# Kernel tuning notes

Measured on AMD Instinct MI355X. Metric: run time of the kernel, lower is better.

The kernel has to match this reference:

```python
import jax, jax.numpy as jnp
import numpy as np

N_HEADS = 16
D_HEAD = 64  # embed_dim // n_heads = 1024 // 16


def setup_inputs() -> dict:
    key = jax.random.key(0)
    ks = jax.random.split(key, 8)
    B, S, E = 2, 2048, 1024
    return {
        "k_in": jax.random.normal(ks[0], (B, S, E), jnp.float32),
        "q_in": jax.random.normal(ks[1], (B, S, E), jnp.float32),
        "v_in": jax.random.normal(ks[2], (B, S, E), jnp.float32),
        "Wq": jax.random.normal(ks[3], (D_HEAD, D_HEAD), jnp.float32) / np.sqrt(D_HEAD),
        "Wk": jax.random.normal(ks[4], (D_HEAD, D_HEAD), jnp.float32) / np.sqrt(D_HEAD),
        "Wv": jax.random.normal(ks[5], (D_HEAD, D_HEAD), jnp.float32) / np.sqrt(D_HEAD),
        "Wo": jax.random.normal(ks[6], (E, E), jnp.float32) / np.sqrt(E),
        "bo": jnp.zeros((E,), jnp.float32),
    }


def reference(k_in, q_in, v_in, Wq, Wk, Wv, Wo, bo):
    B, Sq, E = q_in.shape
    Sk = k_in.shape[1]
    H, Dh = N_HEADS, D_HEAD
    # split heads: [B, S, H, Dh]
    q = q_in.reshape(B, Sq, H, Dh)
    k = k_in.reshape(B, Sk, H, Dh)
    v = v_in.reshape(B, Sk, H, Dh)
    # per-head linear projections (nn.Linear: x @ W.T), then [B, H, S, Dh]
    q = jnp.einsum("bshd,ed->bhse", q, Wq)
    k = jnp.einsum("bshd,ed->bhse", k, Wk)
    v = jnp.einsum("bshd,ed->bhse", v, Wv)
    # scaled dot-product attention
    scores = jnp.einsum("bhqd,bhkd->bhqk", q, k) / jnp.sqrt(jnp.asarray(Dh, q.dtype))
    attn = jax.nn.softmax(scores, axis=-1)
    ctx = jnp.einsum("bhqk,bhkd->bqhd", attn, v)  # [B, Sq, H, Dh]
    concat = ctx.reshape(B, Sq, H * Dh)
    return concat @ Wo.T + bo
```

## Files before the change

kernel.cpp:

```cpp
#include <hip/hip_runtime.h>
#include <hip/hip_fp16.h>

typedef _Float16 f16;
typedef __fp16 hf16x2 __attribute__((ext_vector_type(2)));
typedef _Float16 f16x8 __attribute__((ext_vector_type(8)));
typedef _Float16 f16x4v __attribute__((ext_vector_type(4)));
typedef float f32x4 __attribute__((ext_vector_type(4)));
typedef float f32x16 __attribute__((ext_vector_type(16)));

#define B_ 2
#define S_ 2048
#define E_ 1024
#define H_ 16
#define DH_ 64

__device__ __forceinline__ f32x4 mfma16(f16x8 a, f16x8 b, f32x4 c) {
    return __builtin_amdgcn_mfma_f32_16x16x32_f16(a, b, c, 0, 0, 0);
}
__device__ __forceinline__ f32x16 mfma32(f16x8 a, f16x8 b, f32x16 c) {
    return __builtin_amdgcn_mfma_f32_32x32x16_f16(a, b, c, 0, 0, 0);
}

__device__ __forceinline__ f16x8 cvt8(const float* p) {
    float4 v0 = *(const float4*)p;
    float4 v1 = *(const float4*)(p + 4);
    f16x8 r;
    r[0] = (f16)v0.x; r[1] = (f16)v0.y; r[2] = (f16)v0.z; r[3] = (f16)v0.w;
    r[4] = (f16)v1.x; r[5] = (f16)v1.y; r[6] = (f16)v1.z; r[7] = (f16)v1.w;
    return r;
}

__global__ __launch_bounds__(256) void proj_cvt_kernel(
    const float* __restrict__ q_in, const float* __restrict__ k_in,
    const float* __restrict__ v_in,
    const float* __restrict__ Wq, const float* __restrict__ Wk,
    const float* __restrict__ Wv, const float* __restrict__ Wo,
    f16* __restrict__ Qg, f16* __restrict__ Kg, f16* __restrict__ Vt,
    f16* __restrict__ WoH)
{
    int tid = threadIdx.x;
    int bx = blockIdx.x;
    if (bx >= 3072) {
        int i = (bx - 3072) * 256 + tid;
        float4 v = *(const float4*)(Wo + (size_t)i * 4);
        f16x4v o;
        o[0] = (f16)v.x; o[1] = (f16)v.y; o[2] = (f16)v.z; o[3] = (f16)v.w;
        *(f16x4v*)(WoH + (size_t)i * 4) = o;
        return;
    }

    int lane = tid & 63, wv = tid >> 6;
    int wid = bx * 4 + wv;
    int proj = wid >> 12;
    int r = wid & 4095;
    int bh = r >> 7;
    int stile = r & 127;
    int sbase = stile * 16;
    int h = bh & 15;
    int b = bh >> 4;
    int c = lane & 15, g = lane >> 4;

    const float* x; const float* W;
    if (proj == 0)      { x = q_in; W = Wq; }
    else if (proj == 1) { x = k_in; W = Wk; }
    else                { x = v_in; W = Wv; }

    const float* xrow = x + (((size_t)(b * S_ + sbase + c) * H_ + h) << 6);
    f16x8 a0 = cvt8(xrow + g * 8);
    f16x8 a1 = cvt8(xrow + 32 + g * 8);

    f32x4 acc[4] = {};
#pragma unroll
    for (int nt = 0; nt < 4; ++nt) {
        const float* wrow = W + ((nt * 16 + c) << 6);
        f16x8 b0 = cvt8(wrow + g * 8);
        f16x8 b1 = cvt8(wrow + 32 + g * 8);
        acc[nt] = mfma16(a0, b0, acc[nt]);
        acc[nt] = mfma16(a1, b1, acc[nt]);
    }

    if (proj < 2) {
        f16* out = (proj == 0) ? Qg : Kg;
#pragma unroll
        for (int nt = 0; nt < 4; ++nt)
#pragma unroll
            for (int j = 0; j < 4; ++j) {
                int s = sbase + g * 4 + j;
                out[((size_t)bh * S_ + s) * DH_ + nt * 16 + c] = (f16)acc[nt][j];
            }
    } else {
#pragma unroll
        for (int nt = 0; nt < 4; ++nt) {
            f16x4v pk;
            pk[0] = (f16)acc[nt][0]; pk[1] = (f16)acc[nt][1];
            pk[2] = (f16)acc[nt][2]; pk[3] = (f16)acc[nt][3];
            *(f16x4v*)&Vt[((size_t)bh * DH_ + nt * 16 + c) * S_ + sbase + g * 4] = pk;
        }
    }
}

#define C1_ 0.18033688011112042f

__global__ __launch_bounds__(256, 2) void attn_kernel(
    const f16* __restrict__ Qg, const f16* __restrict__ Kg,
    const f16* __restrict__ Vt, f16* __restrict__ ctx)
{
    __shared__ __align__(16) f16 lds[16384];

    int tid = threadIdx.x, lane = tid & 63, wv = tid >> 6;
    int bid = blockIdx.x;
    int sb = (bid & 7) * 64 + (bid >> 3);
    int bh = sb >> 4, qt = sb & 15;
    int b = bh >> 4, h = bh & 15;
    int qbase = qt * 128 + wv * 32;
    int q32 = lane & 31, hh = lane >> 5;
    bool isLo = (hh == 0);

    const f16* Qh = Qg + (size_t)bh * S_ * DH_;
    const f16* Kh = Kg + (size_t)bh * S_ * DH_;
    const f16* Vh = Vt + (size_t)bh * DH_ * S_;

    int swzr = (q32 & 15) << 3;
    int cr[8];
#pragma unroll
    for (int a = 0; a < 2; ++a)
#pragma unroll
        for (int s = 0; s < 4; ++s)
            cr[4 * a + s] = q32 * 128 + ((a * 64 + 16 * s + 8 * hh) ^ swzr);

    int s0 = tid, s1 = tid + 256;
    int e0 = s0 >> 3, c0 = s0 & 7, e1 = s1 >> 3, c1 = s1 & 7;
    int wd0 = (e0 & 31) * 128 + ((((e0 >> 5) * 64) + c0 * 8) ^ (((e0 & 31) & 15) << 3));
    int wd1 = (e1 & 31) * 128 + ((((e1 >> 5) * 64) + c1 * 8) ^ (((e1 & 31) & 15) << 3));
    const f16* ksp0 = Kh + e0 * 64 + c0 * 8;
    const f16* ksp1 = Kh + e1 * 64 + c1 * 8;
    const f16* vsp0 = Vh + (size_t)e0 * S_ + c0 * 8;
    const f16* vsp1 = Vh + (size_t)e1 * S_ + c1 * 8;

    f16x8 qf[4];
#pragma unroll
    for (int s = 0; s < 4; ++s)
        qf[s] = *(const f16x8*)(Qh + (size_t)(qbase + q32) * DH_ + 16 * s + 8 * hh);

    float m2 = -1e30f, lrv = 0.f;
    f32x16 accO0 = {}, accO1 = {};
    f16x8 kreg0, kreg1, vreg0, vreg1;

    kreg0 = *(const f16x8*)ksp0; kreg1 = *(const f16x8*)ksp1;
    vreg0 = *(const f16x8*)vsp0; vreg1 = *(const f16x8*)vsp1;
    *(f16x8*)&lds[wd0] = kreg0; *(f16x8*)&lds[wd1] = kreg1;
    *(f16x8*)&lds[8192 + wd0] = vreg0; *(f16x8*)&lds[8192 + wd1] = vreg1;
    __syncthreads();

#define ATTN_SUB(CUR, SUBI)                                                    \
    do {                                                                       \
        f32x16 accS = {};                                                      \
        __builtin_amdgcn_s_setprio(1);                                         \
        _Pragma("unroll")                                                      \
        for (int s = 0; s < 4; ++s) {                                          \
            f16x8 kf = *(const f16x8*)&lds[(CUR) * 4096 + cr[4 * (SUBI) + s]]; \
            accS = mfma32(kf, qf[s], accS);                                    \
        }                                                                      \
        __builtin_amdgcn_s_setprio(0);                                         \
        float rmax = accS[0];                                                  \
        _Pragma("unroll")                                                      \
        for (int r = 1; r < 16; ++r) rmax = fmaxf(rmax, accS[r]);              \
        rmax = fmaxf(rmax, __shfl_xor(rmax, 32));                              \
        if (!__all(fmaf(rmax, C1_, -m2) <= 8.f)) {                             \
            float mn = fmaxf(m2, rmax * C1_);                                  \
            float al = exp2f(m2 - mn);                                         \
            m2 = mn; lrv *= al;                                                \
            _Pragma("unroll")                                                  \
            for (int r = 0; r < 16; ++r) {                                     \
                float aj = __shfl(al, ((r & 3) + 8 * (r >> 2)) + 4 * hh);      \
                accO0[r] *= aj; accO1[r] *= aj;                                \
            }                                                                  \
        }                                                                      \
        unsigned w[8];                                                         \
        _Pragma("unroll")                                                      \
        for (int j = 0; j < 8; ++j) {                                          \
            float ea = exp2f(fmaf(accS[2 * j], C1_, -m2));                     \
            float eb = exp2f(fmaf(accS[2 * j + 1], C1_, -m2));                 \
            lrv += ea + eb;                                                    \
            hf16x2 pk = __builtin_amdgcn_cvt_pkrtz(ea, eb);                    \
            w[j] = __builtin_bit_cast(unsigned, pk);                           \
        }                                                                      \
        _Pragma("unroll")                                                      \
        for (int s2 = 0; s2 < 2; ++s2) {                                       \
            unsigned b0 = w[4 * s2 + 0], b1 = w[4 * s2 + 1];                   \
            unsigned b2 = w[4 * s2 + 2], b3 = w[4 * s2 + 3];                   \
            unsigned x0 = (unsigned)__shfl_xor((int)b0, 32);                   \
            unsigned x1 = (unsigned)__shfl_xor((int)b1, 32);                   \
            unsigned x2 = (unsigned)__shfl_xor((int)b2, 32);                   \
            unsigned x3 = (unsigned)__shfl_xor((int)b3, 32);                   \
            uint4 au;                                                          \
            au.x = isLo ? b0 : x2;                                             \
            au.y = isLo ? b1 : x3;                                             \
            au.z = isLo ? x0 : b2;                                             \
            au.w = isLo ? x1 : b3;                                             \
            f16x8 pa = __builtin_bit_cast(f16x8, au);                          \
            __builtin_amdgcn_s_setprio(1);                                     \
            {                                                                  \
                f16x8 vb = *(const f16x8*)&lds[8192 + (CUR) * 4096             \
                                               + cr[(SUBI) * 2 + s2]];         \
                accO0 = mfma32(pa, vb, accO0);                                 \
            }                                                                  \
            {                                                                  \
                f16x8 vb = *(const f16x8*)&lds[8192 + (CUR) * 4096             \
                                               + cr[4 + (SUBI) * 2 + s2]];     \
                accO1 = mfma32(pa, vb, accO1);                                 \
            }                                                                  \
            __builtin_amdgcn_s_setprio(0);                                     \
        }                                                                      \
    } while (0)

#define ATTN_STEP(CUR, T, STAGE)                                               \
    do {                                                                       \
        if (STAGE) {                                                           \
            kreg0 = *(const f16x8*)(ksp0 + ((T) + 1) * 4096);                  \
            kreg1 = *(const f16x8*)(ksp1 + ((T) + 1) * 4096);                  \
            vreg0 = *(const f16x8*)(vsp0 + ((T) + 1) * 64);                    \
            vreg1 = *(const f16x8*)(vsp1 + ((T) + 1) * 64);                    \
        }                                                                      \
        ATTN_SUB(CUR, 0);                                                      \
        ATTN_SUB(CUR, 1);                                                      \
        if (STAGE) {                                                           \
            int nb = (CUR) ^ 1;                                                \
            *(f16x8*)&lds[nb * 4096 + wd0] = kreg0;                            \
            *(f16x8*)&lds[nb * 4096 + wd1] = kreg1;                            \
            *(f16x8*)&lds[8192 + nb * 4096 + wd0] = vreg0;                     \
            *(f16x8*)&lds[8192 + nb * 4096 + wd1] = vreg1;                     \
            __syncthreads();                                                   \
        }                                                                      \
    } while (0)

#pragma unroll 1
    for (int kt = 0; kt < 30; kt += 2) {
        ATTN_STEP(0, kt, 1);
        ATTN_STEP(1, kt + 1, 1);
    }
    ATTN_STEP(0, 30, 1);
    ATTN_STEP(1, 31, 0);
#undef ATTN_STEP
#undef ATTN_SUB

    float lr = lrv + __shfl_xor(lrv, 32);
    float inv = 1.f / lr;
#pragma unroll
    for (int r = 0; r < 16; ++r) {
        int crow = (r & 3) + 8 * (r >> 2);
        float ir = __shfl(inv, crow + 4 * hh);
        int s = qbase + crow + 4 * hh;
        f16* dst = ctx + ((size_t)b * S_ + s) * E_ + h * DH_ + q32;
        dst[0]  = (f16)(accO0[r] * ir);
        dst[32] = (f16)(accO1[r] * ir);
    }
}

__global__ __launch_bounds__(256) void gemm_out(
    const f16* __restrict__ A,
    const f16* __restrict__ Bw,
    const float* __restrict__ bo,
    float* __restrict__ out)
{
    __shared__ __align__(16) f16 Al[2][128 * 64];
    __shared__ __align__(16) f16 Bl[2][64 * 64];

    int tid = threadIdx.x, lane = tid & 63, wv = tid >> 6;
    int bid = blockIdx.x;
    int sb = (bid & 7) * 64 + (bid >> 3);
    int mbase = (sb & 31) * 128, nbase = (sb >> 5) * 64;
    int c = lane & 15, g = lane >> 4;
    int wr = wv >> 1, wc = wv & 1;
    int swz = (c & 7) << 3;

    int adst[4]; const f16* asrc[4];
#pragma unroll
    for (int i = 0; i < 4; ++i) {
        int slot = tid + i * 256;
        int row = slot >> 3, cc = slot & 7;
        adst[i] = row * 64 + ((cc * 8) ^ ((row & 7) << 3));
        asrc[i] = A + (size_t)(mbase + row) * 1024 + cc * 8;
    }
    int bdst[2]; const f16* bsrc[2];
#pragma unroll
    for (int i = 0; i < 2; ++i) {
        int slot = tid + i * 256;
        int row = slot >> 3, cc = slot & 7;
        bdst[i] = row * 64 + ((cc * 8) ^ ((row & 7) << 3));
        bsrc[i] = Bw + (size_t)(nbase + row) * 1024 + cc * 8;
    }

    f32x4 acc[4][2] = {};
    f16x8 areg[4], breg[2];

#pragma unroll
    for (int i = 0; i < 4; ++i) areg[i] = *(const f16x8*)asrc[i];
#pragma unroll
    for (int i = 0; i < 2; ++i) breg[i] = *(const f16x8*)bsrc[i];
#pragma unroll
    for (int i = 0; i < 4; ++i) *(f16x8*)&Al[0][adst[i]] = areg[i];
#pragma unroll
    for (int i = 0; i < 2; ++i) *(f16x8*)&Bl[0][bdst[i]] = breg[i];
    __syncthreads();

#define GEMM_STEP(CUR, T, STAGE)                                               \
    do {                                                                       \
        if (STAGE) {                                                           \
            _Pragma("unroll")                                                  \
            for (int i = 0; i < 4; ++i)                                        \
                areg[i] = *(const f16x8*)(asrc[i] + ((T) + 1) * 64);           \
            _Pragma("unroll")                                                  \
            for (int i = 0; i < 2; ++i)                                        \
                breg[i] = *(const f16x8*)(bsrc[i] + ((T) + 1) * 64);           \
        }                                                                      \
        __builtin_amdgcn_s_setprio(1);                                         \
        _Pragma("unroll")                                                      \
        for (int kk = 0; kk < 2; ++kk) {                                       \
            f16x8 af[4], bf[2];                                                \
            _Pragma("unroll")                                                  \
            for (int mi = 0; mi < 4; ++mi)                                     \
                af[mi] = *(const f16x8*)&Al[CUR][(wr * 64 + mi * 16 + c) * 64  \
                                               + ((32 * kk + 8 * g) ^ swz)];   \
            _Pragma("unroll")                                                  \
            for (int ni = 0; ni < 2; ++ni)                                     \
                bf[ni] = *(const f16x8*)&Bl[CUR][(wc * 32 + ni * 16 + c) * 64  \
                                               + ((32 * kk + 8 * g) ^ swz)];   \
            _Pragma("unroll")                                                  \
            for (int mi = 0; mi < 4; ++mi)                                     \
                _Pragma("unroll")                                              \
                for (int ni = 0; ni < 2; ++ni)                                 \
                    acc[mi][ni] = mfma16(af[mi], bf[ni], acc[mi][ni]);         \
        }                                                                      \
        __builtin_amdgcn_s_setprio(0);                                         \
        if (STAGE) {                                                           \
            int nb = (CUR) ^ 1;                                                \
            _Pragma("unroll")                                                  \
            for (int i = 0; i < 4; ++i) *(f16x8*)&Al[nb][adst[i]] = areg[i];   \
            _Pragma("unroll")                                                  \
            for (int i = 0; i < 2; ++i) *(f16x8*)&Bl[nb][bdst[i]] = breg[i];   \
            __syncthreads();                                                   \
        }                                                                      \
    } while (0)

#pragma unroll 1
    for (int ks = 0; ks < 14; ks += 2) {
        GEMM_STEP(0, ks, 1);
        GEMM_STEP(1, ks + 1, 1);
    }
    GEMM_STEP(0, 14, 1);
    GEMM_STEP(1, 15, 0);
#undef GEMM_STEP

#pragma unroll
    for (int ni = 0; ni < 2; ++ni) {
        float bias = bo[nbase + wc * 32 + ni * 16 + c];
#pragma unroll
        for (int mi = 0; mi < 4; ++mi)
#pragma unroll
            for (int j = 0; j < 4; ++j) {
                int m = mbase + wr * 64 + mi * 16 + g * 4 + j;
                out[(size_t)m * 1024 + nbase + wc * 32 + ni * 16 + c] =
                    acc[mi][ni][j] + bias;
            }
    }
}

extern "C" void kernel_launch(void* const* d_in, const int* in_sizes, int n_in,
                              void* d_out, int out_size, void* d_ws, size_t ws_size,
                              hipStream_t stream)
{
    const float* k_in = (const float*)d_in[0];
    const float* q_in = (const float*)d_in[1];
    const float* v_in = (const float*)d_in[2];
    const float* Wq   = (const float*)d_in[3];
    const float* Wk   = (const float*)d_in[4];
    const float* Wv   = (const float*)d_in[5];
    const float* Wo   = (const float*)d_in[6];
    const float* bo   = (const float*)d_in[7];
    float* out = (float*)d_out;

    char* ws = (char*)d_ws;
    f16* Qg  = (f16*)(ws);
    f16* Kg  = (f16*)(ws + (8u << 20));
    f16* Vt  = (f16*)(ws + (16u << 20));
    f16* ctx = (f16*)(ws + (24u << 20));
    f16* WoH = (f16*)(ws + (32u << 20));

    proj_cvt_kernel<<<dim3(4096), dim3(256), 0, stream>>>(
        q_in, k_in, v_in, Wq, Wk, Wv, Wo, Qg, Kg, Vt, WoH);
    attn_kernel<<<dim3(512), dim3(256), 0, stream>>>(Qg, Kg, Vt, ctx);
    gemm_out<<<dim3(512), dim3(256), 0, stream>>>(ctx, WoH, bo, out);
}
```

Measured before the change: 118.6 us.

## Batch both QK^T sub-tiles before softmax and coalesce Q/K stores via LDS

The attention step now issues the QK^T MFMAs for both 32-key sub-tiles back to back and computes both row maxima together, before running softmax and PV for each. This gives the scheduler more independent MFMA work to overlap with the exp and shuffle sequences, at the cost of holding a second 16-float score accumulator in registers. Separately, the projection kernel stages Q and K results through a small per-wave LDS tile so each lane writes 16-byte contiguous rows instead of scattered 2-byte stores.

```diff
diff --git a/kernel.cpp b/kernel.cpp
--- a/kernel.cpp
+++ b/kernel.cpp
@@ -38,6 +38,8 @@
     f16* __restrict__ Qg, f16* __restrict__ Kg, f16* __restrict__ Vt,
     f16* __restrict__ WoH)
 {
+    __shared__ __align__(16) f16 tr[4][16 * 72];
+
     int tid = threadIdx.x;
     int bx = blockIdx.x;
     if (bx >= 3072) {
@@ -56,8 +58,6 @@
     int bh = r >> 7;
     int stile = r & 127;
     int sbase = stile * 16;
-    int h = bh & 15;
-    int b = bh >> 4;
     int c = lane & 15, g = lane >> 4;
 
     const float* x; const float* W;
@@ -65,36 +65,43 @@
     else if (proj == 1) { x = k_in; W = Wk; }
     else                { x = v_in; W = Wv; }
 
-    const float* xrow = x + (((size_t)(b * S_ + sbase + c) * H_ + h) << 6);
-    f16x8 a0 = cvt8(xrow + g * 8);
-    f16x8 a1 = cvt8(xrow + 32 + g * 8);
-
-    f32x4 acc[4] = {};
-#pragma unroll
-    for (int nt = 0; nt < 4; ++nt) {
-        const float* wrow = W + ((nt * 16 + c) << 6);
-        f16x8 b0 = cvt8(wrow + g * 8);
-        f16x8 b1 = cvt8(wrow + 32 + g * 8);
-        acc[nt] = mfma16(a0, b0, acc[nt]);
-        acc[nt] = mfma16(a1, b1, acc[nt]);
-    }
-
-    if (proj < 2) {
-        f16* out = (proj == 0) ? Qg : Kg;
-#pragma unroll
-        for (int nt = 0; nt < 4; ++nt)
-#pragma unroll
-            for (int j = 0; j < 4; ++j) {
-                int s = sbase + g * 4 + j;
-                out[((size_t)bh * S_ + s) * DH_ + nt * 16 + c] = (f16)acc[nt][j];
+    {
+        int h = bh & 15, b = bh >> 4;
+        const float* xrow = x + (((size_t)(b * S_ + sbase + c) * H_ + h) << 6);
+        f16x8 a0 = cvt8(xrow + g * 8);
+        f16x8 a1 = cvt8(xrow + 32 + g * 8);
+
+        f32x4 acc[4] = {};
+#pragma unroll
+        for (int nt = 0; nt < 4; ++nt) {
+            const float* wrow = W + ((nt * 16 + c) << 6);
+            f16x8 b0 = cvt8(wrow + g * 8);
+            f16x8 b1 = cvt8(wrow + 32 + g * 8);
+            acc[nt] = mfma16(a0, b0, acc[nt]);
+            acc[nt] = mfma16(a1, b1, acc[nt]);
+        }
+
+        if (proj < 2) {
+            f16* out = (proj == 0) ? Qg : Kg;
+            f16* T = &tr[wv][0];
+#pragma unroll
+            for (int nt = 0; nt < 4; ++nt)
+#pragma unroll
+                for (int j = 0; j < 4; ++j)
+                    T[(4 * g + j) * 72 + nt * 16 + c] = (f16)acc[nt][j];
+            int rr = lane >> 3, cc8 = lane & 7;
+            f16x8 r0 = *(const f16x8*)&T[rr * 72 + cc8 * 8];
+            f16x8 r1 = *(const f16x8*)&T[(8 + rr) * 72 + cc8 * 8];
+            *(f16x8*)(out + ((size_t)bh * S_ + sbase + rr) * DH_ + cc8 * 8) = r0;
+            *(f16x8*)(out + ((size_t)bh * S_ + sbase + 8 + rr) * DH_ + cc8 * 8) = r1;
+        } else {
+#pragma unroll
+            for (int nt = 0; nt < 4; ++nt) {
+                f16x4v pk;
+                pk[0] = (f16)acc[nt][0]; pk[1] = (f16)acc[nt][1];
+                pk[2] = (f16)acc[nt][2]; pk[3] = (f16)acc[nt][3];
+                *(f16x4v*)&Vt[((size_t)bh * DH_ + nt * 16 + c) * S_ + sbase + g * 4] = pk;
             }
-    } else {
-#pragma unroll
-        for (int nt = 0; nt < 4; ++nt) {
-            f16x4v pk;
-            pk[0] = (f16)acc[nt][0]; pk[1] = (f16)acc[nt][1];
-            pk[2] = (f16)acc[nt][2]; pk[3] = (f16)acc[nt][3];
-            *(f16x4v*)&Vt[((size_t)bh * DH_ + nt * 16 + c) * S_ + sbase + g * 4] = pk;
         }
     }
 }
@@ -152,22 +159,10 @@
     *(f16x8*)&lds[8192 + wd0] = vreg0; *(f16x8*)&lds[8192 + wd1] = vreg1;
     __syncthreads();
 
-#define ATTN_SUB(CUR, SUBI)                                                    \
+#define SMPV(CUR, SUBI, ACCS, RMAX)                                            \
     do {                                                                       \
-        f32x16 accS = {};                                                      \
-        __builtin_amdgcn_s_setprio(1);                                         \
-        _Pragma("unroll")                                                      \
-        for (int s = 0; s < 4; ++s) {                                          \
-            f16x8 kf = *(const f16x8*)&lds[(CUR) * 4096 + cr[4 * (SUBI) + s]]; \
-            accS = mfma32(kf, qf[s], accS);                                    \
-        }                                                                      \
-        __builtin_amdgcn_s_setprio(0);                                         \
-        float rmax = accS[0];                                                  \
-        _Pragma("unroll")                                                      \
-        for (int r = 1; r < 16; ++r) rmax = fmaxf(rmax, accS[r]);              \
-        rmax = fmaxf(rmax, __shfl_xor(rmax, 32));                              \
-        if (!__all(fmaf(rmax, C1_, -m2) <= 8.f)) {                             \
-            float mn = fmaxf(m2, rmax * C1_);                                  \
+        if (!__all(fmaf(RMAX, C1_, -m2) <= 8.f)) {                             \
+            float mn = fmaxf(m2, (RMAX) * C1_);                                \
             float al = exp2f(m2 - mn);                                         \
             m2 = mn; lrv *= al;                                                \
             _Pragma("unroll")                                                  \
@@ -179,8 +174,8 @@
         unsigned w[8];                                                         \
         _Pragma("unroll")                                                      \
         for (int j = 0; j < 8; ++j) {                                          \
-            float ea = exp2f(fmaf(accS[2 * j], C1_, -m2));                     \
-            float eb = exp2f(fmaf(accS[2 * j + 1], C1_, -m2));                 \
+            float ea = exp2f(fmaf(ACCS[2 * j], C1_, -m2));                     \
+            float eb = exp2f(fmaf(ACCS[2 * j + 1], C1_, -m2));                 \
             lrv += ea + eb;                                                    \
             hf16x2 pk = __builtin_amdgcn_cvt_pkrtz(ea, eb);                    \
             w[j] = __builtin_bit_cast(unsigned, pk);                           \
@@ -222,8 +217,29 @@
             vreg0 = *(const f16x8*)(vsp0 + ((T) + 1) * 64);                    \
             vreg1 = *(const f16x8*)(vsp1 + ((T) + 1) * 64);                    \
         }                                                                      \
-        ATTN_SUB(CUR, 0);                                                      \
-        ATTN_SUB(CUR, 1);                                                      \
+        f32x16 accS0 = {}, accS1 = {};                                         \
+        __builtin_amdgcn_s_setprio(1);                                         \
+        _Pragma("unroll")                                                      \
+        for (int s = 0; s < 4; ++s) {                                          \
+            f16x8 kf = *(const f16x8*)&lds[(CUR) * 4096 + cr[s]];              \
+            accS0 = mfma32(kf, qf[s], accS0);                                  \
+        }                                                                      \
+        _Pragma("unroll")                                                      \
+        for (int s = 0; s < 4; ++s) {                                          \
+            f16x8 kf = *(const f16x8*)&lds[(CUR) * 4096 + cr[4 + s]];          \
+            accS1 = mfma32(kf, qf[s], accS1);                                  \
+        }                                                                      \
+        __builtin_amdgcn_s_setprio(0);                                         \
+        float rmax0 = accS0[0], rmax1 = accS1[0];                              \
+        _Pragma("unroll")                                                      \
+        for (int r = 1; r < 16; ++r) {                                         \
+            rmax0 = fmaxf(rmax0, accS0[r]);                                    \
+            rmax1 = fmaxf(rmax1, accS1[r]);                                    \
+        }                                                                      \
+        rmax0 = fmaxf(rmax0, __shfl_xor(rmax0, 32));                           \
+        rmax1 = fmaxf(rmax1, __shfl_xor(rmax1, 32));                           \
+        SMPV(CUR, 0, accS0, rmax0);                                            \
+        SMPV(CUR, 1, accS1, rmax1);                                            \
         if (STAGE) {                                                           \
             int nb = (CUR) ^ 1;                                                \
             *(f16x8*)&lds[nb * 4096 + wd0] = kreg0;                            \
@@ -242,7 +258,7 @@
     ATTN_STEP(0, 30, 1);
     ATTN_STEP(1, 31, 0);
 #undef ATTN_STEP
-#undef ATTN_SUB
+#undef SMPV
 
     float lr = lrv + __shfl_xor(lrv, 32);
     float inv = 1.f / lr;
```

Measured after the change: 117.9 us. Within noise of the previous version (-0.6%).
